# Optimization experiments

Measured on AMD Instinct MI355X. Metric: run time of the kernel, lower is better.

The kernel has to match this reference:

```python
import jax, jax.numpy as jnp
import numpy as np

N_NODES = 50000
N_EDGES = 1600000
N_FEATURES = 1433
HIDDEN = 256
N_CLASSES = 7


def setup_inputs() -> dict:
    key = jax.random.key(0)
    ks = jax.random.split(key, 5)
    x = jax.random.normal(ks[0], (N_NODES, N_FEATURES), dtype=jnp.float32)
    edge_index = jax.random.randint(ks[1], (2, N_EDGES), 0, N_NODES, dtype=jnp.int64)
    # Glorot-style init like PyG's Linear inside GCNConv
    W1 = jax.random.normal(ks[2], (N_FEATURES, HIDDEN), dtype=jnp.float32) * (1.0 / np.sqrt(N_FEATURES))
    b1 = jnp.zeros((HIDDEN,), dtype=jnp.float32)
    W2 = jax.random.normal(ks[3], (HIDDEN, N_CLASSES), dtype=jnp.float32) * (1.0 / np.sqrt(HIDDEN))
    b2 = jnp.zeros((N_CLASSES,), dtype=jnp.float32)
    return {"x": x, "edge_index": edge_index, "W1": W1, "b1": b1, "W2": W2, "b2": b2}


def _gcn_conv(x, W, b, src, dst, n_nodes):
    """PyG GCNConv: add self-loops, symmetric deg^{-1/2} norm, linear, scatter-add, +bias."""
    h = x @ W  # [N, out]
    loop = jnp.arange(n_nodes, dtype=src.dtype)
    src2 = jnp.concatenate([src, loop])
    dst2 = jnp.concatenate([dst, loop])
    ones = jnp.ones(src2.shape[0], dtype=h.dtype)
    deg = jax.ops.segment_sum(ones, dst2, num_segments=n_nodes)
    dinv = jnp.where(deg > 0, jax.lax.rsqrt(deg), 0.0)
    norm = dinv[src2] * dinv[dst2]  # [E+N]
    msg = h[src2] * norm[:, None]   # gather + scale
    out = jax.ops.segment_sum(msg, dst2, num_segments=n_nodes)
    return out + b


def reference(x, edge_index, W1, b1, W2, b2):
    src, dst = edge_index[0], edge_index[1]
    h = _gcn_conv(x, W1, b1, src, dst, N_NODES)
    h = jax.nn.relu(h)
    # dropout p=0.5 is identity in eval mode (training=False)
    out = _gcn_conv(h, W2, b2, src, dst, N_NODES)
    return out
```

## Files before the change

### kernel.cpp

```cpp
#include <hip/hip_runtime.h>
#include <hip/hip_bf16.h>


#define N_NODES_   50000
#define NB_ROWS_   50048
#define N_EDGES_   1600000
#define N_FEAT_    1433
#define K_PAD_     1440
#define HIDDEN_    256
#define N_CLASSES_ 7
#define NPART_     ((N_NODES_ + 255) / 256)
#define NT_        (K_PAD_ / 32)

typedef __attribute__((ext_vector_type(8))) short short8;
typedef __attribute__((ext_vector_type(8))) unsigned short ushort8;
typedef __attribute__((ext_vector_type(4))) float f32x4;
typedef unsigned int u32;
typedef unsigned short u16;

__device__ __forceinline__ u16 f2bf(float f) {
    __hip_bfloat16 h = __float2bfloat16(f);
    return *(u16*)&h;
}
__device__ __forceinline__ float bf2f(u16 u) {
    return __uint_as_float((u32)u << 16);
}
__device__ __forceinline__ void global_to_lds16(const void* g, void* l) {
    __builtin_amdgcn_global_load_lds(
        (const __attribute__((address_space(1))) u32*)g,
        (__attribute__((address_space(3))) u32*)l, 16, 0, 0);
}

__global__ void deg_kernel(const int* __restrict__ dst, int* __restrict__ deg) {
    int i = blockIdx.x * blockDim.x + threadIdx.x;
    if (i < N_EDGES_) atomicAdd(&deg[dst[i]], 1);
}

__global__ void dinv_kernel(const int* __restrict__ deg, float* __restrict__ dinv) {
    int i = blockIdx.x * blockDim.x + threadIdx.x;
    if (i < N_NODES_) dinv[i] = rsqrtf((float)(deg[i] + 1));
}

__global__ __launch_bounds__(256) void scan1_kernel(const int* __restrict__ deg,
                                                    int* __restrict__ partial) {
    __shared__ int ws[4];
    int t = threadIdx.x, b = blockIdx.x;
    int idx = b * 256 + t;
    int v = (idx < N_NODES_) ? deg[idx] : 0;
    #pragma unroll
    for (int off = 32; off > 0; off >>= 1) v += __shfl_down(v, off, 64);
    if ((t & 63) == 0) ws[t >> 6] = v;
    __syncthreads();
    if (t == 0) partial[b] = ws[0] + ws[1] + ws[2] + ws[3];
}

__global__ __launch_bounds__(256) void scan2_kernel(int* __restrict__ partial,
                                                    int* __restrict__ blk_off) {
    __shared__ int sh[256];
    int t = threadIdx.x;
    int v = (t < NPART_) ? partial[t] : 0;
    sh[t] = v;
    __syncthreads();
    #pragma unroll
    for (int off = 1; off < 256; off <<= 1) {
        int a = (t >= off) ? sh[t - off] : 0;
        __syncthreads();
        sh[t] += a;
        __syncthreads();
    }
    if (t < NPART_) blk_off[t] = sh[t] - v;
}

__global__ __launch_bounds__(256) void scan3_kernel(const int* __restrict__ deg,
                                                    const int* __restrict__ blk_off,
                                                    int* __restrict__ row_ptr,
                                                    int* __restrict__ cursor) {
    __shared__ int sh[256];
    int t = threadIdx.x, b = blockIdx.x;
    int idx = b * 256 + t;
    int v = (idx < N_NODES_) ? deg[idx] : 0;
    sh[t] = v;
    __syncthreads();
    #pragma unroll
    for (int off = 1; off < 256; off <<= 1) {
        int a = (t >= off) ? sh[t - off] : 0;
        __syncthreads();
        sh[t] += a;
        __syncthreads();
    }
    if (idx < N_NODES_) {
        int rp = blk_off[b] + sh[t] - v;
        row_ptr[idx] = rp;
        cursor[idx]  = rp;
    }
    if (idx == 0) row_ptr[N_NODES_] = N_EDGES_;
}

__global__ void csr_scatter_kernel(const int* __restrict__ src, const int* __restrict__ dst,
                                   int* __restrict__ cursor, int* __restrict__ csr_src) {
    int i = blockIdx.x * blockDim.x + threadIdx.x;
    if (i >= N_EDGES_) return;
    int d = dst[i];
    int pos = atomicAdd(&cursor[d], 1);
    csr_src[pos] = src[i];
}

__global__ void w1t_kernel(const float* __restrict__ W1, u16* __restrict__ W1T) {
    int gid = blockIdx.x * blockDim.x + threadIdx.x;
    if (gid >= HIDDEN_ * K_PAD_) return;
    int k = gid % K_PAD_, n = gid / K_PAD_;
    float v = (k < N_FEAT_) ? W1[(long)k * HIDDEN_ + n] : 0.f;
    W1T[(long)n * K_PAD_ + k] = f2bf(v);
}

__global__ __launch_bounds__(256) void gemm1_fused(const float* __restrict__ X,
                                                   const u16* __restrict__ BT,
                                                   const float* __restrict__ dinv,
                                                   u16* __restrict__ C) {
    __shared__ u16 As[2 * 32 * 32];
    __shared__ u16 Bs[2 * 256 * 32];

    const int tid  = threadIdx.x;
    const int lane = tid & 63;
    const int wv   = tid >> 6;
    const int row0 = blockIdx.x * 32;

    f32x4 acc[2][4] = {};

    const int ar = tid >> 5;
    const int ak = tid & 31;
    const int awc = (ak >> 3);
    const int awo = (ak & 7);
    const int srow = lane >> 2;
    const int ch   = lane & 3;
    const int fm = lane & 15;
    const int q  = lane >> 4;

    float av[4];

    #pragma unroll
    for (int j = 0; j < 4; j++) {
        int rcl = min(row0 + ar + 8 * j, N_NODES_ - 1);
        av[j] = X[(long)rcl * N_FEAT_ + ak];
    }
    #pragma unroll
    for (int j = 0; j < 4; j++) {
        int rb = j * 64 + wv * 16;
        int r  = rb + srow;
        int c  = ch ^ ((r >> 1) & 3);
        global_to_lds16(BT + (long)r * K_PAD_ + 8 * c, &Bs[rb * 32]);
    }
    #pragma unroll
    for (int j = 0; j < 4; j++) {
        int r = ar + 8 * j;
        As[r * 32 + ((awc ^ ((r >> 1) & 3)) << 3) + awo] = f2bf(av[j]);
    }
    __syncthreads();

    int buf = 0;
    for (int t = 0; t < NT_ - 1; ++t) {
        const int k0n = (t + 1) * 32;
        int kcl = min(k0n + ak, N_FEAT_ - 1);
        #pragma unroll
        for (int j = 0; j < 4; j++) {
            int rcl = min(row0 + ar + 8 * j, N_NODES_ - 1);
            av[j] = X[(long)rcl * N_FEAT_ + kcl];
        }
        #pragma unroll
        for (int j = 0; j < 4; j++) {
            int rb = j * 64 + wv * 16;
            int r  = rb + srow;
            int c  = ch ^ ((r >> 1) & 3);
            global_to_lds16(BT + (long)r * K_PAD_ + k0n + 8 * c,
                            &Bs[(buf ^ 1) * 8192 + rb * 32]);
        }
        short8 af[2], bfr[4];
        #pragma unroll
        for (int mi = 0; mi < 2; mi++) {
            int ra = mi * 16 + fm;
            af[mi] = *(const short8*)&As[buf * 1024 + ra * 32 + ((q ^ ((ra >> 1) & 3)) << 3)];
        }
        #pragma unroll
        for (int ni = 0; ni < 4; ni++) {
            int rb2 = wv * 64 + ni * 16 + fm;
            bfr[ni] = *(const short8*)&Bs[buf * 8192 + rb2 * 32 + ((q ^ ((rb2 >> 1) & 3)) << 3)];
        }
        #pragma unroll
        for (int mi = 0; mi < 2; mi++)
            #pragma unroll
            for (int ni = 0; ni < 4; ni++)
                acc[mi][ni] = __builtin_amdgcn_mfma_f32_16x16x32_bf16(af[mi], bfr[ni], acc[mi][ni], 0, 0, 0);
        __builtin_amdgcn_sched_barrier(0);
        #pragma unroll
        for (int j = 0; j < 4; j++) {
            int r = ar + 8 * j;
            As[(buf ^ 1) * 1024 + r * 32 + ((awc ^ ((r >> 1) & 3)) << 3) + awo] = f2bf(av[j]);
        }
        __syncthreads();
        buf ^= 1;
    }

    {
        short8 af[2], bfr[4];
        #pragma unroll
        for (int mi = 0; mi < 2; mi++) {
            int ra = mi * 16 + fm;
            af[mi] = *(const short8*)&As[buf * 1024 + ra * 32 + ((q ^ ((ra >> 1) & 3)) << 3)];
        }
        #pragma unroll
        for (int ni = 0; ni < 4; ni++) {
            int rb2 = wv * 64 + ni * 16 + fm;
            bfr[ni] = *(const short8*)&Bs[buf * 8192 + rb2 * 32 + ((q ^ ((rb2 >> 1) & 3)) << 3)];
        }
        #pragma unroll
        for (int mi = 0; mi < 2; mi++)
            #pragma unroll
            for (int ni = 0; ni < 4; ni++)
                acc[mi][ni] = __builtin_amdgcn_mfma_f32_16x16x32_bf16(af[mi], bfr[ni], acc[mi][ni], 0, 0, 0);
    }

    const int q4 = (lane >> 4) * 4;
    #pragma unroll
    for (int mi = 0; mi < 2; mi++) {
        #pragma unroll
        for (int r = 0; r < 4; r++) {
            int gm = row0 + mi * 16 + q4 + r;
            if (gm < N_NODES_) {
                float sc = dinv[gm];
                #pragma unroll
                for (int ni = 0; ni < 4; ni++) {
                    int gn = wv * 64 + ni * 16 + fm;
                    C[(long)gm * HIDDEN_ + gn] = f2bf(acc[mi][ni][r] * sc);
                }
            }
        }
    }
}

__global__ __launch_bounds__(256) void agg_gemm2_kernel(const u16* __restrict__ h1s,
                                                        const int* __restrict__ row_ptr,
                                                        const int* __restrict__ csr_src,
                                                        const float* __restrict__ dinv,
                                                        const float* __restrict__ b1,
                                                        const float* __restrict__ W2,
                                                        float* __restrict__ h2s) {
    __shared__ float w2s[HIDDEN_ * N_CLASSES_];
    __shared__ float b1s[HIDDEN_];
    int tid = threadIdx.x;
    for (int i = tid; i < HIDDEN_ * N_CLASSES_; i += 256) w2s[i] = W2[i];
    for (int i = tid; i < HIDDEN_; i += 256) b1s[i] = b1[i];
    __syncthreads();

    int wave = tid >> 6;
    int lane = tid & 63;
    int node = blockIdx.x * 4 + wave;
    if (node >= N_NODES_) return;

    int e0 = row_ptr[node], e1 = row_ptr[node + 1];
    float ax = 0.f, ay = 0.f, az = 0.f, aw = 0.f;

    int sL = (e0 + lane < e1) ? csr_src[e0 + lane] : N_NODES_;
    for (int base = e0; base < e1; base += 64) {
        int sCur = sL;
        int nb = base + 64;
        if (nb < e1) sL = (nb + lane < e1) ? csr_src[nb + lane] : N_NODES_;
        int cnt8 = (min(64, e1 - base) + 7) & ~7;
        for (int j = 0; j < cnt8; j += 8) {
            #pragma unroll
            for (int t = 0; t < 8; t++) {
                int s = __shfl(sCur, j + t, 64);
                ushort4 u = ((const ushort4*)(h1s + (long)s * HIDDEN_))[lane];
                ax += bf2f(u.x);
                ay += bf2f(u.y);
                az += bf2f(u.z);
                aw += bf2f(u.w);
            }
        }
    }
    float nd = dinv[node];
    ushort4 su = ((const ushort4*)(h1s + (long)node * HIDDEN_))[lane];
    float xv[4];
    xv[0] = fmaxf((ax + bf2f(su.x)) * nd + b1s[lane * 4 + 0], 0.f);
    xv[1] = fmaxf((ay + bf2f(su.y)) * nd + b1s[lane * 4 + 1], 0.f);
    xv[2] = fmaxf((az + bf2f(su.z)) * nd + b1s[lane * 4 + 2], 0.f);
    xv[3] = fmaxf((aw + bf2f(su.w)) * nd + b1s[lane * 4 + 3], 0.f);

    float p[N_CLASSES_];
    #pragma unroll
    for (int c = 0; c < N_CLASSES_; c++) {
        float a = 0.f;
        #pragma unroll
        for (int i = 0; i < 4; i++)
            a += xv[i] * w2s[(lane * 4 + i) * N_CLASSES_ + c];
        p[c] = a;
    }
    #pragma unroll
    for (int off = 32; off > 0; off >>= 1)
        #pragma unroll
        for (int c = 0; c < N_CLASSES_; c++)
            p[c] += __shfl_down(p[c], off, 64);
    if (lane == 0) {
        #pragma unroll
        for (int c = 0; c < N_CLASSES_; c++)
            h2s[(long)node * 8 + c] = p[c] * nd;
    }
}

__global__ void out_kernel(const float* __restrict__ h2s,
                           const int* __restrict__ row_ptr,
                           const int* __restrict__ csr_src,
                           const float* __restrict__ dinv,
                           const float* __restrict__ b2,
                           float* __restrict__ out) {
    long gid = (long)blockIdx.x * blockDim.x + threadIdx.x;
    int node = (int)(gid >> 3);
    int c = (int)(gid & 7);
    if (node >= N_NODES_ || c >= N_CLASSES_) return;
    int e0 = row_ptr[node], e1 = row_ptr[node + 1];
    float acc = 0.f;
    for (int e = e0; e < e1; e += 4) {
        int s0 = csr_src[e];
        int s1 = (e + 1 < e1) ? csr_src[e + 1] : N_NODES_;
        int s2 = (e + 2 < e1) ? csr_src[e + 2] : N_NODES_;
        int s3 = (e + 3 < e1) ? csr_src[e + 3] : N_NODES_;
        float v0 = h2s[(long)s0 * 8 + c];
        float v1 = h2s[(long)s1 * 8 + c];
        float v2 = h2s[(long)s2 * 8 + c];
        float v3 = h2s[(long)s3 * 8 + c];
        acc += (v0 + v1) + (v2 + v3);
    }
    float nd = dinv[node];
    out[(long)node * N_CLASSES_ + c] =
        (acc + h2s[(long)node * 8 + c]) * nd + b2[c];
}

extern "C" void kernel_launch(void* const* d_in, const int* in_sizes, int n_in,
                              void* d_out, int out_size, void* d_ws, size_t ws_size,
                              hipStream_t stream) {
    const float* x   = (const float*)d_in[0];
    const int*   ei  = (const int*)d_in[1];
    const int*   src = ei;
    const int*   dst = ei + N_EDGES_;
    const float* W1  = (const float*)d_in[2];
    const float* b1  = (const float*)d_in[3];
    const float* W2  = (const float*)d_in[4];
    const float* b2  = (const float*)d_in[5];
    float* out = (float*)d_out;

    char* ws = (char*)d_ws;
    size_t off = 0;
    auto alloc = [&](size_t bytes) { void* p = ws + off; off = (off + bytes + 255) & ~(size_t)255; return p; };
    u16*   h1s     = (u16*)alloc((size_t)(N_NODES_ + 1) * HIDDEN_ * 2);
    u16*   w1t     = (u16*)alloc((size_t)HIDDEN_ * K_PAD_ * 2);
    float* h2s     = (float*)alloc((size_t)(N_NODES_ + 1) * 8 * 4);
    int*   deg     = (int*)alloc((size_t)N_NODES_ * 4);
    float* dinv    = (float*)alloc((size_t)N_NODES_ * 4);
    int*   row_ptr = (int*)alloc((size_t)(N_NODES_ + 1) * 4);
    int*   cursor  = (int*)alloc((size_t)N_NODES_ * 4);
    int*   csr_src = (int*)alloc((size_t)N_EDGES_ * 4);
    int*   partial = (int*)alloc((size_t)NPART_ * 4);
    int*   blk_off = (int*)alloc((size_t)NPART_ * 4);

    hipMemsetAsync(deg, 0, (size_t)N_NODES_ * 4, stream);
    hipMemsetAsync(h1s + (size_t)N_NODES_ * HIDDEN_, 0, HIDDEN_ * 2, stream);
    hipMemsetAsync(h2s + (size_t)N_NODES_ * 8, 0, 8 * 4, stream);

    deg_kernel<<<(N_EDGES_ + 255) / 256, 256, 0, stream>>>(dst, deg);
    dinv_kernel<<<(N_NODES_ + 255) / 256, 256, 0, stream>>>(deg, dinv);
    scan1_kernel<<<NPART_, 256, 0, stream>>>(deg, partial);
    scan2_kernel<<<1, 256, 0, stream>>>(partial, blk_off);
    scan3_kernel<<<NPART_, 256, 0, stream>>>(deg, blk_off, row_ptr, cursor);
    csr_scatter_kernel<<<(N_EDGES_ + 255) / 256, 256, 0, stream>>>(src, dst, cursor, csr_src);

    w1t_kernel<<<(HIDDEN_ * K_PAD_ + 255) / 256, 256, 0, stream>>>(W1, w1t);

    gemm1_fused<<<NB_ROWS_ / 32, 256, 0, stream>>>(x, w1t, dinv, h1s);

    agg_gemm2_kernel<<<(N_NODES_ + 3) / 4, 256, 0, stream>>>(h1s, row_ptr, csr_src, dinv, b1, W2, h2s);

    long out_threads = (long)N_NODES_ * 8;
    out_kernel<<<(unsigned)((out_threads + 255) / 256), 256, 0, stream>>>(h2s, row_ptr, csr_src, dinv, b2, out);
}
```

Baseline: 828.5 us.

## Load W1 fragments directly from global memory instead of staging through LDS

The gemm1 kernel no longer stages the B (W1 transposed) tile into a double-buffered LDS array with global_load_lds. Each wave now reads its short8 B fragments straight from global memory (relying on L2/cache, since W1T is small and shared by all blocks). This removes a 32 KB LDS allocation, which can raise occupancy, and also drops the LDS write/read traffic and a sched_barrier. The cost is that B loads are no longer prefetched one tile ahead, so global-memory latency now sits directly in front of the MFMAs.

After: 855.9 us. 3.3% more time.

```diff
diff --git a/kernel.cpp b/kernel.cpp
--- a/kernel.cpp
+++ b/kernel.cpp
@@ -25,11 +25,6 @@
 __device__ __forceinline__ float bf2f(u16 u) {
     return __uint_as_float((u32)u << 16);
 }
-__device__ __forceinline__ void global_to_lds16(const void* g, void* l) {
-    __builtin_amdgcn_global_load_lds(
-        (const __attribute__((address_space(1))) u32*)g,
-        (__attribute__((address_space(3))) u32*)l, 16, 0, 0);
-}
 
 __global__ void deg_kernel(const int* __restrict__ dst, int* __restrict__ deg) {
     int i = blockIdx.x * blockDim.x + threadIdx.x;
@@ -118,7 +113,6 @@
                                                    const float* __restrict__ dinv,
                                                    u16* __restrict__ C) {
     __shared__ u16 As[2 * 32 * 32];
-    __shared__ u16 Bs[2 * 256 * 32];
 
     const int tid  = threadIdx.x;
     const int lane = tid & 63;
@@ -131,10 +125,10 @@
     const int ak = tid & 31;
     const int awc = (ak >> 3);
     const int awo = (ak & 7);
-    const int srow = lane >> 2;
-    const int ch   = lane & 3;
     const int fm = lane & 15;
     const int q  = lane >> 4;
+
+    const u16* bbase = BT + (long)(wv * 64 + fm) * K_PAD_ + q * 8;
 
     float av[4];
 
@@ -145,13 +139,6 @@
     }
     #pragma unroll
     for (int j = 0; j < 4; j++) {
-        int rb = j * 64 + wv * 16;
-        int r  = rb + srow;
-        int c  = ch ^ ((r >> 1) & 3);
-        global_to_lds16(BT + (long)r * K_PAD_ + 8 * c, &Bs[rb * 32]);
-    }
-    #pragma unroll
-    for (int j = 0; j < 4; j++) {
         int r = ar + 8 * j;
         As[r * 32 + ((awc ^ ((r >> 1) & 3)) << 3) + awo] = f2bf(av[j]);
     }
@@ -159,38 +146,29 @@
 
     int buf = 0;
     for (int t = 0; t < NT_ - 1; ++t) {
-        const int k0n = (t + 1) * 32;
+        const int k0  = t * 32;
+        const int k0n = k0 + 32;
         int kcl = min(k0n + ak, N_FEAT_ - 1);
         #pragma unroll
         for (int j = 0; j < 4; j++) {
             int rcl = min(row0 + ar + 8 * j, N_NODES_ - 1);
             av[j] = X[(long)rcl * N_FEAT_ + kcl];
         }
-        #pragma unroll
-        for (int j = 0; j < 4; j++) {
-            int rb = j * 64 + wv * 16;
-            int r  = rb + srow;
-            int c  = ch ^ ((r >> 1) & 3);
-            global_to_lds16(BT + (long)r * K_PAD_ + k0n + 8 * c,
-                            &Bs[(buf ^ 1) * 8192 + rb * 32]);
-        }
-        short8 af[2], bfr[4];
+        short8 bfr[4];
+        #pragma unroll
+        for (int ni = 0; ni < 4; ni++)
+            bfr[ni] = *(const short8*)(bbase + (long)ni * 16 * K_PAD_ + k0);
+        short8 af[2];
         #pragma unroll
         for (int mi = 0; mi < 2; mi++) {
             int ra = mi * 16 + fm;
             af[mi] = *(const short8*)&As[buf * 1024 + ra * 32 + ((q ^ ((ra >> 1) & 3)) << 3)];
-        }
-        #pragma unroll
-        for (int ni = 0; ni < 4; ni++) {
-            int rb2 = wv * 64 + ni * 16 + fm;
-            bfr[ni] = *(const short8*)&Bs[buf * 8192 + rb2 * 32 + ((q ^ ((rb2 >> 1) & 3)) << 3)];
         }
         #pragma unroll
         for (int mi = 0; mi < 2; mi++)
             #pragma unroll
             for (int ni = 0; ni < 4; ni++)
                 acc[mi][ni] = __builtin_amdgcn_mfma_f32_16x16x32_bf16(af[mi], bfr[ni], acc[mi][ni], 0, 0, 0);
-        __builtin_amdgcn_sched_barrier(0);
         #pragma unroll
         for (int j = 0; j < 4; j++) {
             int r = ar + 8 * j;
@@ -201,16 +179,16 @@
     }
 
     {
-        short8 af[2], bfr[4];
+        const int k0 = (NT_ - 1) * 32;
+        short8 bfr[4];
+        #pragma unroll
+        for (int ni = 0; ni < 4; ni++)
+            bfr[ni] = *(const short8*)(bbase + (long)ni * 16 * K_PAD_ + k0);
+        short8 af[2];
         #pragma unroll
         for (int mi = 0; mi < 2; mi++) {
             int ra = mi * 16 + fm;
             af[mi] = *(const short8*)&As[buf * 1024 + ra * 32 + ((q ^ ((ra >> 1) & 3)) << 3)];
-        }
-        #pragma unroll
-        for (int ni = 0; ni < 4; ni++) {
-            int rb2 = wv * 64 + ni * 16 + fm;
-            bfr[ni] = *(const short8*)&Bs[buf * 8192 + rb2 * 32 + ((q ^ ((rb2 >> 1) & 3)) << 3)];
         }
         #pragma unroll
         for (int mi = 0; mi < 2; mi++)
```
